# Optimization experiments

Measured on AMD Instinct MI355X. Metric: run time of the kernel, lower is better.

Reference implementation:

```python
import jax, jax.numpy as jnp
import numpy as np

B, S, H = 8, 4096, 1024
NUM_WORDS = 8192

def setup_inputs() -> dict:
    key = jax.random.key(0)
    k1, k2 = jax.random.split(key)
    hidden_states = jax.random.normal(k1, (B, S, H), dtype=jnp.float32)
    # contiguous ragged word segments over the flattened token stream,
    # equivalent to per-batch (start, end) word boundaries
    segment_ids = jnp.sort(jax.random.randint(k2, (B * S,), 0, NUM_WORDS)).astype(jnp.int32)
    return {"hidden_states": hidden_states, "segment_ids": segment_ids, "num_segments": NUM_WORDS}

def reference(hidden_states, segment_ids, num_segments):
    # hidden_states: [B, S, H]; segment_ids: [B*S] token -> word id
    tokens = hidden_states.reshape(-1, hidden_states.shape[-1])  # [B*S, H]
    sums = jax.ops.segment_sum(tokens, segment_ids, num_segments=num_segments)  # [W, H]
    counts = jax.ops.segment_sum(jnp.ones((tokens.shape[0],), dtype=tokens.dtype),
                                 segment_ids, num_segments=num_segments)  # [W]
    # average pooling per word; empty segments (count==0) are guarded like the
    # original's `continue` (they would simply not appear; here they are zeros)
    pooled = sums / jnp.maximum(counts, 1.0)[:, None]
    return pooled  # [total_words, H]
```

## Files before the change

### kernel.cpp

```cpp
#include <hip/hip_runtime.h>
#include <hip/hip_bf16.h>


__device__ __forceinline__ int lower_bound_i32(const int* __restrict__ a, int n, int val) {
    int lo = 0, hi = n;
    while (lo < hi) {
        int mid = (lo + hi) >> 1;
        if (a[mid] < val) lo = mid + 1;
        else hi = mid;
    }
    return lo;
}

__global__ __launch_bounds__(256)
void word_pool_kernel(const float* __restrict__ hs,
                      const int* __restrict__ seg,
                      float* __restrict__ out,
                      int n_tokens, int H) {
    const int w = blockIdx.x;

    const int start = lower_bound_i32(seg, n_tokens, w);
    const int end   = lower_bound_i32(seg, n_tokens, w + 1);

    const int h = threadIdx.x * 4;
    if (h >= H) return;

    float4 acc = make_float4(0.f, 0.f, 0.f, 0.f);
    for (int t = start; t < end; ++t) {
        const float4 v = *reinterpret_cast<const float4*>(&hs[(size_t)t * H + h]);
        acc.x += v.x; acc.y += v.y; acc.z += v.z; acc.w += v.w;
    }

    const int cnt = end - start;
    const float inv = (cnt > 0) ? (1.0f / (float)cnt) : 0.0f;
    acc.x *= inv; acc.y *= inv; acc.z *= inv; acc.w *= inv;

    *reinterpret_cast<float4*>(&out[(size_t)w * H + h]) = acc;
}

extern "C" void kernel_launch(void* const* d_in, const int* in_sizes, int n_in,
                              void* d_out, int out_size, void* d_ws, size_t ws_size,
                              hipStream_t stream) {
    const float* hs  = (const float*)d_in[0];
    const int*   seg = (const int*)d_in[1];
    float* out = (float*)d_out;

    const int n_tokens = in_sizes[1];
    const int H        = in_sizes[0] / n_tokens;
    const int n_words  = out_size / H;

    dim3 grid(n_words);
    dim3 block(256);
    word_pool_kernel<<<grid, block, 0, stream>>>(hs, seg, out, n_tokens, H);
}
```

Measured before the change: 34.96 us.

## Precompute word start offsets in a separate kernel instead of per-block binary search

Adds a pre-pass kernel that scans adjacent segment ids and writes the start token index for every word into workspace. The pooling kernel then reads two offsets rather than doing two dependent binary searches over the segment array. This removes serialized global-load latency at block start, at the cost of an extra kernel launch and workspace traffic.

```diff
diff --git a/kernel.cpp b/kernel.cpp
--- a/kernel.cpp
+++ b/kernel.cpp
@@ -2,25 +2,27 @@
 #include <hip/hip_bf16.h>
 
 
-__device__ __forceinline__ int lower_bound_i32(const int* __restrict__ a, int n, int val) {
-    int lo = 0, hi = n;
-    while (lo < hi) {
-        int mid = (lo + hi) >> 1;
-        if (a[mid] < val) lo = mid + 1;
-        else hi = mid;
+__global__ __launch_bounds__(256)
+void word_bounds_kernel(const int* __restrict__ seg,
+                        int* __restrict__ starts,
+                        int n_tokens, int n_words) {
+    const int t = blockIdx.x * blockDim.x + threadIdx.x;
+    if (t > n_tokens) return;
+    const int prev = (t == 0) ? -1 : seg[t - 1];
+    const int cur  = (t == n_tokens) ? n_words : seg[t];
+    for (int w = prev + 1; w <= cur; ++w) {
+        starts[w] = t;
     }
-    return lo;
 }
 
 __global__ __launch_bounds__(256)
 void word_pool_kernel(const float* __restrict__ hs,
-                      const int* __restrict__ seg,
+                      const int* __restrict__ starts,
                       float* __restrict__ out,
-                      int n_tokens, int H) {
+                      int H) {
     const int w = blockIdx.x;
-
-    const int start = lower_bound_i32(seg, n_tokens, w);
-    const int end   = lower_bound_i32(seg, n_tokens, w + 1);
+    const int start = starts[w];
+    const int end   = starts[w + 1];
 
     const int h = threadIdx.x * 4;
     if (h >= H) return;
@@ -49,7 +51,15 @@
     const int H        = in_sizes[0] / n_tokens;
     const int n_words  = out_size / H;
 
-    dim3 grid(n_words);
-    dim3 block(256);
-    word_pool_kernel<<<grid, block, 0, stream>>>(hs, seg, out, n_tokens, H);
+    int* starts = (int*)d_ws;
+
+    {
+        const int total = n_tokens + 1;
+        dim3 grid((total + 255) / 256), block(256);
+        word_bounds_kernel<<<grid, block, 0, stream>>>(seg, starts, n_tokens, n_words);
+    }
+    {
+        dim3 grid(n_words), block(256);
+        word_pool_kernel<<<grid, block, 0, stream>>>(hs, starts, out, H);
+    }
 }
```

Result: slower. 36.10 us (+3.3%).
